# Kernel tuning notes

Measured on AMD Instinct MI355X. Metric: run time of the kernel, lower is better.

Reference implementation:

```python
import jax, jax.numpy as jnp
import numpy as np

N_NODES = 100000
N_EDGES = 1600000
D_IN, D_HID, D_OUT = 128, 128, 64


def setup_inputs() -> dict:
    key = jax.random.key(0)
    ks = jax.random.split(key, 6)
    x = jax.random.normal(ks[0], (N_NODES, D_IN), dtype=jnp.float32)
    edge_index = jax.random.randint(ks[1], (2, N_EDGES), 0, N_NODES, dtype=jnp.int64)
    s1 = 1.0 / np.sqrt(D_IN)
    s2 = 1.0 / np.sqrt(D_HID)
    return {
        "x": x,
        "edge_index": edge_index,
        "Wl1": jax.random.uniform(ks[2], (D_HID, D_IN), jnp.float32, -s1, s1),
        "bl1": jnp.zeros((D_HID,), jnp.float32),
        "Wr1": jax.random.uniform(ks[3], (D_HID, D_IN), jnp.float32, -s1, s1),
        "Wl2": jax.random.uniform(ks[4], (D_OUT, D_HID), jnp.float32, -s2, s2),
        "bl2": jnp.zeros((D_OUT,), jnp.float32),
        "Wr2": jax.random.uniform(ks[5], (D_OUT, D_HID), jnp.float32, -s2, s2),
    }


def _sage_conv(x, src, dst, Wl, bl, Wr, n_nodes):
    # mean-aggregate neighbor features src -> dst
    agg = jax.ops.segment_sum(x[src], dst, num_segments=n_nodes)  # [N, d_in]
    deg = jax.ops.segment_sum(jnp.ones((src.shape[0],), x.dtype), dst, num_segments=n_nodes)
    agg = agg / jnp.maximum(deg, 1.0)[:, None]
    # PyG SAGEConv: lin_l(agg) + lin_r(x), bias only on lin_l
    return agg @ Wl.T + bl + x @ Wr.T


def reference(x, edge_index, Wl1, bl1, Wr1, Wl2, bl2, Wr2):
    src, dst = edge_index[0], edge_index[1]
    n = x.shape[0]
    h = _sage_conv(x, src, dst, Wl1, bl1, Wr1, n)
    h = jax.nn.relu(h)
    # dropout is identity in eval mode (training=False)
    out = _sage_conv(h, src, dst, Wl2, bl2, Wr2, n)
    return out
```

## Files before the change

### kernel.cpp

```cpp
#include <hip/hip_runtime.h>

#define N_NODES_C 100000
#define N_EDGES_C 1600000
#define NT32_C 3125
#define NBUCK_C 392
#define BCAP_C 4800
#define EPB_C 2048
#define HCAP_C 2816

typedef _Float16 half_t;
typedef __attribute__((ext_vector_type(2))) _Float16 half2v;
typedef __attribute__((ext_vector_type(8))) _Float16 half8v;
typedef __attribute__((ext_vector_type(4))) float floatx4;

#if defined(__has_builtin)
#if __has_builtin(__builtin_amdgcn_fdot2)
#define HAS_FDOT2 1
#endif
#endif

__launch_bounds__(512, 2)
__global__ void bucket_kernel(const int* __restrict__ src, const int* __restrict__ dst,
                              int* __restrict__ gcur, int* __restrict__ bucket, int E) {
    __shared__ int eord[EPB_C];
    __shared__ unsigned short obkt[EPB_C];
    __shared__ int lcnt[512];
    __shared__ int lcur[512];
    __shared__ int lbase[512];
    __shared__ int sc[2][512];
    const int tid = threadIdx.x;
    const int e0 = blockIdx.x * EPB_C;
    const int n = min(EPB_C, E - e0);

    lcnt[tid] = 0;
    lcur[tid] = 0;
    __syncthreads();
    int ent[4];
    int bk[4];
#pragma unroll
    for (int u = 0; u < 4; u++) {
        int i = u * 512 + tid;
        bk[u] = -1;
        if (i < n) {
            int d = dst[e0 + i];
            int s = src[e0 + i];
            int b = d >> 8;
            ent[u] = (s << 8) | (d & 255);
            bk[u] = b;
            atomicAdd(&lcnt[b], 1);
        }
    }
    __syncthreads();
    sc[0][tid] = lcnt[tid];
    __syncthreads();
    int cur = 0;
    for (int off = 1; off < 512; off <<= 1) {
        int v = sc[cur][tid] + ((tid >= off) ? sc[cur][tid - off] : 0);
        sc[1 - cur][tid] = v;
        __syncthreads();
        cur ^= 1;
    }
    for (int i = tid; i < NBUCK_C; i += 512) {
        int c = lcnt[i];
        lbase[i] = (c > 0) ? atomicAdd(&gcur[i], c) : 0;
    }
    __syncthreads();
#pragma unroll
    for (int u = 0; u < 4; u++) {
        int b = bk[u];
        if (b >= 0) {
            int slot = atomicAdd(&lcur[b], 1);
            int pos = (sc[cur][b] - lcnt[b]) + slot;
            eord[pos] = ent[u];
            obkt[pos] = (unsigned short)b;
        }
    }
    __syncthreads();
    for (int i = tid; i < n; i += 512) {
        int b = obkt[i];
        int pre = sc[cur][b] - lcnt[b];
        int gpos = lbase[b] + (i - pre);
        if (gpos < BCAP_C) bucket[b * BCAP_C + gpos] = eord[i];
    }
}

__launch_bounds__(512, 2)
__global__ void csr_build_kernel(const int* __restrict__ gcur, const int* __restrict__ bucket,
                                 int2* __restrict__ nodeinfo, int* __restrict__ csr, int N) {
    __shared__ int lcnt[256];
    __shared__ int lcur[128];
    __shared__ int sc[2][512];
    __shared__ int eord[HCAP_C];
    __shared__ int bbase_sh;
    const int b = blockIdx.x >> 1;
    const int hf = blockIdx.x & 1;
    const int tid = threadIdx.x;

    int v = (tid < NBUCK_C) ? min(gcur[tid], BCAP_C) : 0;
    sc[0][tid] = v;
    if (tid < 256) lcnt[tid] = 0;
    if (tid < 128) lcur[tid] = 0;
    __syncthreads();
    int cur = 0;
    for (int off = 1; off < 512; off <<= 1) {
        int nv = sc[cur][tid] + ((tid >= off) ? sc[cur][tid - off] : 0);
        sc[1 - cur][tid] = nv;
        __syncthreads();
        cur ^= 1;
    }
    if (tid == 0) bbase_sh = (b == 0) ? 0 : sc[cur][b - 1];
    const int ne = min(gcur[b], BCAP_C);
    const int* be = bucket + b * BCAP_C;

    int pv[10];
#pragma unroll
    for (int u = 0; u < 10; u++) {
        int i = u * 512 + tid;
        pv[u] = -1;
        if (i < ne) {
            int p = be[i];
            pv[u] = p;
            atomicAdd(&lcnt[p & 255], 1);
        }
    }
    __syncthreads();

    if (tid < 256) sc[0][tid] = lcnt[tid];
    __syncthreads();
    cur = 0;
    for (int off = 1; off < 256; off <<= 1) {
        int nv = 0;
        if (tid < 256) nv = sc[cur][tid] + ((tid >= off) ? sc[cur][tid - off] : 0);
        if (tid < 256) sc[1 - cur][tid] = nv;
        __syncthreads();
        cur ^= 1;
    }
    const int j0 = hf * 128;
    const int pre0 = (j0 == 0) ? 0 : sc[cur][j0 - 1];
    const int L = min(sc[cur][j0 + 127] - pre0, HCAP_C);
#pragma unroll
    for (int u = 0; u < 10; u++) {
        int p = pv[u];
        if (p >= 0) {
            int j = p & 255;
            if ((j >> 7) == hf) {
                int slot = atomicAdd(&lcur[j - j0], 1);
                int idx = (sc[cur][j] - lcnt[j]) - pre0 + slot;
                if (idx < HCAP_C) eord[idx] = p >> 8;
            }
        }
    }
    __syncthreads();
    const int gb = bbase_sh + pre0;
    for (int i = tid; i < L; i += 512) csr[gb + i] = eord[i];
    if (tid < 128) {
        int node = (b << 8) + j0 + tid;
        if (node < N) {
            int j = j0 + tid;
            nodeinfo[node] = make_int2(bbase_sh + (sc[cur][j] - lcnt[j]), lcnt[j]);
        }
    }
}

__global__ void prep_kernel(const float* __restrict__ Wl1, const float* __restrict__ Wr1,
                            const float* __restrict__ Wl2, const float* __restrict__ Wr2,
                            const float* __restrict__ x,
                            half_t* __restrict__ B1, half_t* __restrict__ B2,
                            half_t* __restrict__ xh, int* __restrict__ gcur) {
    int blk = blockIdx.x;
    int tid = threadIdx.x;
    if (blk == 0 && tid < 196) { gcur[tid] = 0; gcur[tid + 196] = 0; }
    if (blk < 128) {
        int t = blk * 256 + tid;
        int j  = t & 7;
        int l  = (t >> 3) & 63;
        int ks = (t >> 9) & 7;
        int ct = t >> 12;
        int k = ks * 32 + ((l >> 4) << 3) + j;
        int o = ct * 16 + (l & 15);
        float v = (k < 128) ? Wl1[o * 128 + k] : Wr1[o * 128 + (k - 128)];
        B1[t] = (half_t)v;
    } else if (blk < 192) {
        int t = (blk - 128) * 256 + tid;
        int j  = t & 7;
        int l  = (t >> 3) & 63;
        int ks = (t >> 9) & 3;
        int ct = t >> 11;
        int k = ks * 32 + ((l >> 4) << 3) + j;
        int o = ct * 16 + (l & 15);
        float v = (o < 64) ? Wl2[o * 128 + k] : Wr2[(o - 64) * 128 + k];
        B2[t] = (half_t)v;
    } else {
        int t = (blk - 192) * 256 + tid;
        if (t >= N_NODES_C * 16) return;
        const float4* p = (const float4*)x;
        float4 a = p[(size_t)t * 2];
        float4 b = p[(size_t)t * 2 + 1];
        half_t r[8] = {(half_t)a.x, (half_t)a.y, (half_t)a.z, (half_t)a.w,
                       (half_t)b.x, (half_t)b.y, (half_t)b.z, (half_t)b.w};
        *(uint4*)(xh + (size_t)t * 8) = *(uint4*)r;
    }
}

static __device__ __forceinline__ void dot8(float* a, uint4 v) {
    unsigned int u[4] = {v.x, v.y, v.z, v.w};
#ifdef HAS_FDOT2
    const half2v e0 = {(half_t)1.0f, (half_t)0.0f};
    const half2v e1 = {(half_t)0.0f, (half_t)1.0f};
#pragma unroll
    for (int i = 0; i < 4; i++) {
        union { unsigned int x; half2v h; } c; c.x = u[i];
        a[2 * i]     = __builtin_amdgcn_fdot2(c.h, e0, a[2 * i], false);
        a[2 * i + 1] = __builtin_amdgcn_fdot2(c.h, e1, a[2 * i + 1], false);
    }
#else
#pragma unroll
    for (int i = 0; i < 4; i++) {
        union { unsigned int x; half2v h; } c; c.x = u[i];
        a[2 * i]     += (float)c.h.x;
        a[2 * i + 1] += (float)c.h.y;
    }
#endif
}

__global__ void agg1_kernel(const half_t* __restrict__ xh,
                            const int2* __restrict__ nodeinfo,
                            const int* __restrict__ csr,
                            half_t* __restrict__ aggh, int N) {
    int wid = (blockIdx.x * 256 + threadIdx.x) >> 6;
    if (wid >= N) return;
    int lane = threadIdx.x & 63;
    int q = lane >> 4;
    int c = lane & 15;
    int2 info = nodeinfo[wid];
    const int* row = csr + info.x;
    const int deg = info.y;
    float a0[8] = {0,0,0,0,0,0,0,0};
    float a1[8] = {0,0,0,0,0,0,0,0};
    int e = q;
    for (; e + 12 < deg; e += 16) {
        int s0 = row[e];
        int s1 = row[e + 4];
        int s2 = row[e + 8];
        int s3 = row[e + 12];
        uint4 v0 = *(const uint4*)(xh + (size_t)s0 * 128 + c * 8);
        uint4 v1 = *(const uint4*)(xh + (size_t)s1 * 128 + c * 8);
        uint4 v2 = *(const uint4*)(xh + (size_t)s2 * 128 + c * 8);
        uint4 v3 = *(const uint4*)(xh + (size_t)s3 * 128 + c * 8);
        dot8(a0, v0);
        dot8(a1, v1);
        dot8(a0, v2);
        dot8(a1, v3);
    }
    for (; e + 4 < deg; e += 8) {
        int s0 = row[e];
        int s1 = row[e + 4];
        uint4 v0 = *(const uint4*)(xh + (size_t)s0 * 128 + c * 8);
        uint4 v1 = *(const uint4*)(xh + (size_t)s1 * 128 + c * 8);
        dot8(a0, v0);
        dot8(a1, v1);
    }
    if (e < deg) {
        uint4 v0 = *(const uint4*)(xh + (size_t)row[e] * 128 + c * 8);
        dot8(a0, v0);
    }
    float acc[8];
#pragma unroll
    for (int j = 0; j < 8; j++) {
        float v = a0[j] + a1[j];
        v += __shfl_xor(v, 16, 64);
        v += __shfl_xor(v, 32, 64);
        acc[j] = v;
    }
    if (lane < 16) {
        float sc = 1.0f / fmaxf((float)deg, 1.0f);
        half_t r[8];
#pragma unroll
        for (int j = 0; j < 8; j++) r[j] = (half_t)(acc[j] * sc);
        *(uint4*)(aggh + (size_t)wid * 128 + c * 8) = *(uint4*)r;
    }
}

__launch_bounds__(256, 2)
__global__ void gemm12_kernel(const half_t* __restrict__ aggh,
                              const half_t* __restrict__ xh,
                              const half_t* __restrict__ B1,
                              const float* __restrict__ bias1,
                              const half_t* __restrict__ B2,
                              const float* __restrict__ bias2,
                              half_t* __restrict__ g,
                              half_t* __restrict__ s2h) {
    __shared__ half_t sA[32][264];
    __shared__ half_t sH[32][136];

    const int wave = threadIdx.x >> 6;
    const int lane = threadIdx.x & 63;
    const int quad = lane >> 4;
    const int l16 = lane & 15;
    const int tid = threadIdx.x;

    half8v bf1[2][8];
    float bv1[2];
    half8v bf2[2][4];
    float bv2[2];
#pragma unroll
    for (int i = 0; i < 2; i++) {
        int ct = wave * 2 + i;
        bv1[i] = bias1[ct * 16 + l16];
        int o = ct * 16 + l16;
        bv2[i] = (o >= 64) ? bias2[o - 64] : 0.f;
#pragma unroll
        for (int ks = 0; ks < 8; ks++)
            bf1[i][ks] = *(const half8v*)(B1 + ((ct * 8 + ks) * 64 + lane) * 8);
#pragma unroll
        for (int ks = 0; ks < 4; ks++)
            bf2[i][ks] = *(const half8v*)(B2 + ((ct * 4 + ks) * 64 + lane) * 8);
    }

    for (int tile = blockIdx.x; tile < NT32_C; tile += gridDim.x) {
        const int node0 = tile * 32;
        for (int u = tid; u < 512; u += 256) {
            int n = u >> 4, cc = u & 15;
            *(half8v*)&sA[n][cc * 8] =
                *(const half8v*)(aggh + (size_t)(node0 + n) * 128 + cc * 8);
            *(half8v*)&sA[n][128 + cc * 8] =
                *(const half8v*)(xh + (size_t)(node0 + n) * 128 + cc * 8);
        }
        __syncthreads();

        floatx4 acc[2][2];
#pragma unroll
        for (int i = 0; i < 2; i++)
#pragma unroll
            for (int s = 0; s < 2; s++)
                acc[i][s] = (floatx4){0.f, 0.f, 0.f, 0.f};
#pragma unroll
        for (int ks = 0; ks < 8; ks++) {
            half8v a0 = *(const half8v*)&sA[l16][ks * 32 + quad * 8];
            half8v a1 = *(const half8v*)&sA[16 + l16][ks * 32 + quad * 8];
#pragma unroll
            for (int i = 0; i < 2; i++) {
                acc[i][0] = __builtin_amdgcn_mfma_f32_16x16x32_f16(a0, bf1[i][ks], acc[i][0], 0, 0, 0);
                acc[i][1] = __builtin_amdgcn_mfma_f32_16x16x32_f16(a1, bf1[i][ks], acc[i][1], 0, 0, 0);
            }
        }
#pragma unroll
        for (int i = 0; i < 2; i++) {
            int o = wave * 32 + i * 16 + l16;
#pragma unroll
            for (int s = 0; s < 2; s++) {
                float vals[4] = {acc[i][s].x, acc[i][s].y, acc[i][s].z, acc[i][s].w};
#pragma unroll
                for (int r = 0; r < 4; r++) {
                    int n = s * 16 + quad * 4 + r;
                    sH[n][o] = (half_t)fmaxf(vals[r] + bv1[i], 0.f);
                }
            }
        }
        __syncthreads();

#pragma unroll
        for (int i = 0; i < 2; i++)
#pragma unroll
            for (int s = 0; s < 2; s++)
                acc[i][s] = (floatx4){0.f, 0.f, 0.f, 0.f};
#pragma unroll
        for (int ks = 0; ks < 4; ks++) {
            half8v a0 = *(const half8v*)&sH[l16][ks * 32 + quad * 8];
            half8v a1 = *(const half8v*)&sH[16 + l16][ks * 32 + quad * 8];
#pragma unroll
            for (int i = 0; i < 2; i++) {
                acc[i][0] = __builtin_amdgcn_mfma_f32_16x16x32_f16(a0, bf2[i][ks], acc[i][0], 0, 0, 0);
                acc[i][1] = __builtin_amdgcn_mfma_f32_16x16x32_f16(a1, bf2[i][ks], acc[i][1], 0, 0, 0);
            }
        }
#pragma unroll
        for (int i = 0; i < 2; i++) {
            int o = wave * 32 + i * 16 + l16;
#pragma unroll
            for (int s = 0; s < 2; s++) {
                float vals[4] = {acc[i][s].x, acc[i][s].y, acc[i][s].z, acc[i][s].w};
#pragma unroll
                for (int r = 0; r < 4; r++) {
                    int node = node0 + s * 16 + quad * 4 + r;
                    float v = vals[r] + bv2[i];
                    if (o < 64) g[(size_t)node * 64 + o] = (half_t)v;
                    else        s2h[(size_t)node * 64 + (o - 64)] = (half_t)v;
                }
            }
        }
        __syncthreads();
    }
}

__global__ void agg2e_kernel(const half_t* __restrict__ g,
                             const half_t* __restrict__ s2h,
                             const int2* __restrict__ nodeinfo,
                             const int* __restrict__ csr,
                             float* __restrict__ out, int N) {
    int wid = (blockIdx.x * 256 + threadIdx.x) >> 6;
    if (wid >= N) return;
    int lane = threadIdx.x & 63;
    int q = lane >> 3;
    int c = lane & 7;
    int2 info = nodeinfo[wid];
    const int* row = csr + info.x;
    const int deg = info.y;
    float a0[8] = {0,0,0,0,0,0,0,0};
    float a1[8] = {0,0,0,0,0,0,0,0};
    int e = q;
    for (; e + 8 < deg; e += 16) {
        int s0 = row[e];
        int s1 = row[e + 8];
        uint4 v0 = *(const uint4*)(g + (size_t)s0 * 64 + c * 8);
        uint4 v1 = *(const uint4*)(g + (size_t)s1 * 64 + c * 8);
        dot8(a0, v0);
        dot8(a1, v1);
    }
    if (e < deg) {
        uint4 v0 = *(const uint4*)(g + (size_t)row[e] * 64 + c * 8);
        dot8(a0, v0);
    }
    float acc[8];
#pragma unroll
    for (int j = 0; j < 8; j++) {
        float v = a0[j] + a1[j];
        v += __shfl_xor(v, 8, 64);
        v += __shfl_xor(v, 16, 64);
        v += __shfl_xor(v, 32, 64);
        acc[j] = v;
    }
    if (lane < 8) {
        float sc = 1.0f / fmaxf((float)deg, 1.0f);
        uint4 sv = *(const uint4*)(s2h + (size_t)wid * 64 + c * 8);
        union { unsigned int x; half2v h; } c0, c1, c2, c3;
        c0.x = sv.x; c1.x = sv.y; c2.x = sv.z; c3.x = sv.w;
        float4 r0, r1;
        r0.x = acc[0] * sc + (float)c0.h.x;
        r0.y = acc[1] * sc + (float)c0.h.y;
        r0.z = acc[2] * sc + (float)c1.h.x;
        r0.w = acc[3] * sc + (float)c1.h.y;
        r1.x = acc[4] * sc + (float)c2.h.x;
        r1.y = acc[5] * sc + (float)c2.h.y;
        r1.z = acc[6] * sc + (float)c3.h.x;
        r1.w = acc[7] * sc + (float)c3.h.y;
        *(float4*)(out + (size_t)wid * 64 + c * 8) = r0;
        *(float4*)(out + (size_t)wid * 64 + c * 8 + 4) = r1;
    }
}

extern "C" void kernel_launch(void* const* d_in, const int* in_sizes, int n_in,
                              void* d_out, int out_size, void* d_ws, size_t ws_size,
                              hipStream_t stream) {
    const float* x    = (const float*)d_in[0];
    const int*   ei   = (const int*)d_in[1];
    const float* Wl1  = (const float*)d_in[2];
    const float* bl1  = (const float*)d_in[3];
    const float* Wr1  = (const float*)d_in[4];
    const float* Wl2  = (const float*)d_in[5];
    const float* bl2  = (const float*)d_in[6];
    const float* Wr2  = (const float*)d_in[7];
    float* out = (float*)d_out;

    const int N = N_NODES_C;
    const int E = N_EDGES_C;
    const int* src = ei;
    const int* dst = ei + E;

    char* ws = (char*)d_ws;
    half_t* B1   = (half_t*)(ws + 0);
    half_t* B2   = (half_t*)(ws + 65536);
    int*    gcur = (int*)   (ws + 98304);
    int2*   nodeinfo = (int2*)(ws + 102400);
    int*    csr  = (int*)   (ws + 1048576);
    half_t* xh   = (half_t*)(ws + 7448576);
    half_t* g    = (half_t*)(ws + 33048576);
    half_t* s2h  = g + 6400000;
    half_t* aggh = (half_t*)(ws + 58648576);
    int*    bucket = (int*)aggh;

    prep_kernel<<<192 + (N * 16 + 255) / 256, 256, 0, stream>>>(
        Wl1, Wr1, Wl2, Wr2, x, B1, B2, xh, gcur);
    bucket_kernel<<<(E + EPB_C - 1) / EPB_C, 512, 0, stream>>>(src, dst, gcur, bucket, E);
    csr_build_kernel<<<NBUCK_C * 2, 512, 0, stream>>>(gcur, bucket, nodeinfo, csr, N);
    agg1_kernel<<<(N + 3) / 4, 256, 0, stream>>>(xh, nodeinfo, csr, aggh, N);
    gemm12_kernel<<<512, 256, 0, stream>>>(aggh, xh, B1, bl1, B2, bl2, g, s2h);
    agg2e_kernel<<<(N + 3) / 4, 256, 0, stream>>>(g, s2h, nodeinfo, csr, out, N);
}
```

Before: 258.6 us.

## Fuse prep conversion into bucket kernel and build CSR per whole bucket

The weight/feature fp16 conversion blocks are appended to the edge-bucketing launch so both run in one kernel, and the gcur counters are zeroed with a memset instead. The CSR build now uses one block per bucket instead of two half-bucket blocks, so the histogram and prefix scan are no longer computed twice and the HCAP truncation is gone. In exchange each block holds a larger shared eord buffer (BCAP entries), which may lower occupancy, and there are half as many blocks. It also adds a memset call on the stream.

```diff
diff --git a/kernel.cpp b/kernel.cpp
--- a/kernel.cpp
+++ b/kernel.cpp
@@ -6,7 +6,7 @@
 #define NBUCK_C 392
 #define BCAP_C 4800
 #define EPB_C 2048
-#define HCAP_C 2816
+#define NBB_C 782
 
 typedef _Float16 half_t;
 typedef __attribute__((ext_vector_type(2))) _Float16 half2v;
@@ -20,8 +20,13 @@
 #endif
 
 __launch_bounds__(512, 2)
-__global__ void bucket_kernel(const int* __restrict__ src, const int* __restrict__ dst,
-                              int* __restrict__ gcur, int* __restrict__ bucket, int E) {
+__global__ void prepbucket_kernel(const int* __restrict__ src, const int* __restrict__ dst,
+                                  int* __restrict__ gcur, int* __restrict__ bucket, int E,
+                                  const float* __restrict__ Wl1, const float* __restrict__ Wr1,
+                                  const float* __restrict__ Wl2, const float* __restrict__ Wr2,
+                                  const float* __restrict__ x,
+                                  half_t* __restrict__ B1, half_t* __restrict__ B2,
+                                  half_t* __restrict__ xh) {
     __shared__ int eord[EPB_C];
     __shared__ unsigned short obkt[EPB_C];
     __shared__ int lcnt[512];
@@ -29,6 +34,42 @@
     __shared__ int lbase[512];
     __shared__ int sc[2][512];
     const int tid = threadIdx.x;
+
+    if (blockIdx.x >= NBB_C) {
+        int blk = blockIdx.x - NBB_C;
+        if (blk < 64) {
+            int t = blk * 512 + tid;
+            int j  = t & 7;
+            int l  = (t >> 3) & 63;
+            int ks = (t >> 9) & 7;
+            int ct = t >> 12;
+            int k = ks * 32 + ((l >> 4) << 3) + j;
+            int o = ct * 16 + (l & 15);
+            float v = (k < 128) ? Wl1[o * 128 + k] : Wr1[o * 128 + (k - 128)];
+            B1[t] = (half_t)v;
+        } else if (blk < 96) {
+            int t = (blk - 64) * 512 + tid;
+            int j  = t & 7;
+            int l  = (t >> 3) & 63;
+            int ks = (t >> 9) & 3;
+            int ct = t >> 11;
+            int k = ks * 32 + ((l >> 4) << 3) + j;
+            int o = ct * 16 + (l & 15);
+            float v = (o < 64) ? Wl2[o * 128 + k] : Wr2[(o - 64) * 128 + k];
+            B2[t] = (half_t)v;
+        } else {
+            int t = (blk - 96) * 512 + tid;
+            if (t >= N_NODES_C * 16) return;
+            const float4* p = (const float4*)x;
+            float4 a = p[(size_t)t * 2];
+            float4 b = p[(size_t)t * 2 + 1];
+            half_t r[8] = {(half_t)a.x, (half_t)a.y, (half_t)a.z, (half_t)a.w,
+                           (half_t)b.x, (half_t)b.y, (half_t)b.z, (half_t)b.w};
+            *(uint4*)(xh + (size_t)t * 8) = *(uint4*)r;
+        }
+        return;
+    }
+
     const int e0 = blockIdx.x * EPB_C;
     const int n = min(EPB_C, E - e0);
 
@@ -88,18 +129,16 @@
 __global__ void csr_build_kernel(const int* __restrict__ gcur, const int* __restrict__ bucket,
                                  int2* __restrict__ nodeinfo, int* __restrict__ csr, int N) {
     __shared__ int lcnt[256];
-    __shared__ int lcur[128];
+    __shared__ int lcur[256];
     __shared__ int sc[2][512];
-    __shared__ int eord[HCAP_C];
+    __shared__ int eord[BCAP_C];
     __shared__ int bbase_sh;
-    const int b = blockIdx.x >> 1;
-    const int hf = blockIdx.x & 1;
+    const int b = blockIdx.x;
     const int tid = threadIdx.x;
 
     int v = (tid < NBUCK_C) ? min(gcur[tid], BCAP_C) : 0;
     sc[0][tid] = v;
-    if (tid < 256) lcnt[tid] = 0;
-    if (tid < 128) lcur[tid] = 0;
+    if (tid < 256) { lcnt[tid] = 0; lcur[tid] = 0; }
     __syncthreads();
     int cur = 0;
     for (int off = 1; off < 512; off <<= 1) {
@@ -135,70 +174,24 @@
         __syncthreads();
         cur ^= 1;
     }
-    const int j0 = hf * 128;
-    const int pre0 = (j0 == 0) ? 0 : sc[cur][j0 - 1];
-    const int L = min(sc[cur][j0 + 127] - pre0, HCAP_C);
 #pragma unroll
     for (int u = 0; u < 10; u++) {
         int p = pv[u];
         if (p >= 0) {
             int j = p & 255;
-            if ((j >> 7) == hf) {
-                int slot = atomicAdd(&lcur[j - j0], 1);
-                int idx = (sc[cur][j] - lcnt[j]) - pre0 + slot;
-                if (idx < HCAP_C) eord[idx] = p >> 8;
-            }
-        }
-    }
-    __syncthreads();
-    const int gb = bbase_sh + pre0;
-    for (int i = tid; i < L; i += 512) csr[gb + i] = eord[i];
-    if (tid < 128) {
-        int node = (b << 8) + j0 + tid;
+            int slot = atomicAdd(&lcur[j], 1);
+            int idx = (sc[cur][j] - lcnt[j]) + slot;
+            eord[idx] = p >> 8;
+        }
+    }
+    __syncthreads();
+    const int gb = bbase_sh;
+    for (int i = tid; i < ne; i += 512) csr[gb + i] = eord[i];
+    if (tid < 256) {
+        int node = (b << 8) + tid;
         if (node < N) {
-            int j = j0 + tid;
-            nodeinfo[node] = make_int2(bbase_sh + (sc[cur][j] - lcnt[j]), lcnt[j]);
-        }
-    }
-}
-
-__global__ void prep_kernel(const float* __restrict__ Wl1, const float* __restrict__ Wr1,
-                            const float* __restrict__ Wl2, const float* __restrict__ Wr2,
-                            const float* __restrict__ x,
-                            half_t* __restrict__ B1, half_t* __restrict__ B2,
-                            half_t* __restrict__ xh, int* __restrict__ gcur) {
-    int blk = blockIdx.x;
-    int tid = threadIdx.x;
-    if (blk == 0 && tid < 196) { gcur[tid] = 0; gcur[tid + 196] = 0; }
-    if (blk < 128) {
-        int t = blk * 256 + tid;
-        int j  = t & 7;
-        int l  = (t >> 3) & 63;
-        int ks = (t >> 9) & 7;
-        int ct = t >> 12;
-        int k = ks * 32 + ((l >> 4) << 3) + j;
-        int o = ct * 16 + (l & 15);
-        float v = (k < 128) ? Wl1[o * 128 + k] : Wr1[o * 128 + (k - 128)];
-        B1[t] = (half_t)v;
-    } else if (blk < 192) {
-        int t = (blk - 128) * 256 + tid;
-        int j  = t & 7;
-        int l  = (t >> 3) & 63;
-        int ks = (t >> 9) & 3;
-        int ct = t >> 11;
-        int k = ks * 32 + ((l >> 4) << 3) + j;
-        int o = ct * 16 + (l & 15);
-        float v = (o < 64) ? Wl2[o * 128 + k] : Wr2[(o - 64) * 128 + k];
-        B2[t] = (half_t)v;
-    } else {
-        int t = (blk - 192) * 256 + tid;
-        if (t >= N_NODES_C * 16) return;
-        const float4* p = (const float4*)x;
-        float4 a = p[(size_t)t * 2];
-        float4 b = p[(size_t)t * 2 + 1];
-        half_t r[8] = {(half_t)a.x, (half_t)a.y, (half_t)a.z, (half_t)a.w,
-                       (half_t)b.x, (half_t)b.y, (half_t)b.z, (half_t)b.w};
-        *(uint4*)(xh + (size_t)t * 8) = *(uint4*)r;
+            nodeinfo[node] = make_int2(gb + (sc[cur][tid] - lcnt[tid]), lcnt[tid]);
+        }
     }
 }
 
@@ -479,10 +472,10 @@
     half_t* aggh = (half_t*)(ws + 58648576);
     int*    bucket = (int*)aggh;
 
-    prep_kernel<<<192 + (N * 16 + 255) / 256, 256, 0, stream>>>(
-        Wl1, Wr1, Wl2, Wr2, x, B1, B2, xh, gcur);
-    bucket_kernel<<<(E + EPB_C - 1) / EPB_C, 512, 0, stream>>>(src, dst, gcur, bucket, E);
-    csr_build_kernel<<<NBUCK_C * 2, 512, 0, stream>>>(gcur, bucket, nodeinfo, csr, N);
+    hipMemsetAsync(gcur, 0, NBUCK_C * sizeof(int), stream);
+    prepbucket_kernel<<<NBB_C + 96 + (N_NODES_C * 16) / 512, 512, 0, stream>>>(
+        src, dst, gcur, bucket, E, Wl1, Wr1, Wl2, Wr2, x, B1, B2, xh);
+    csr_build_kernel<<<NBUCK_C, 512, 0, stream>>>(gcur, bucket, nodeinfo, csr, N);
     agg1_kernel<<<(N + 3) / 4, 256, 0, stream>>>(xh, nodeinfo, csr, aggh, N);
     gemm12_kernel<<<512, 256, 0, stream>>>(aggh, xh, B1, bl1, B2, bl2, g, s2h);
     agg2e_kernel<<<(N + 3) / 4, 256, 0, stream>>>(g, s2h, nodeinfo, csr, out, N);
```

Result: no change. 255.3 us (-1.3%).
